# Performance work log

Hardware: AMD Instinct MI355X
Metric: run time of the kernel (lower is better)

## Reference

```python
import jax, jax.numpy as jnp
import numpy as np
from jax import lax

V = 10475
J = 55
B = 512
# Kinematic tree: hardcoded chain (parent[i] = i-1), root = 0.
PARENTS = np.concatenate([[-1], np.arange(J - 1)]).astype(np.int32)


def rodrigues(r):
    """Axis-angle (..., 3) -> rotation matrices (..., 3, 3)."""
    angle = jnp.sqrt(jnp.sum(r * r, axis=-1, keepdims=True) + 1e-12)  # (...,1)
    axis = r / angle
    s = jnp.sin(angle)[..., None]
    c = jnp.cos(angle)[..., None]
    kx, ky, kz = axis[..., 0], axis[..., 1], axis[..., 2]
    z = jnp.zeros_like(kx)
    K = jnp.stack([z, -kz, ky, kz, z, -kx, -ky, kx, z], axis=-1).reshape(r.shape[:-1] + (3, 3))
    I = jnp.eye(3, dtype=r.dtype)
    return I + s * K + (1.0 - c) * (K @ K)


def setup_inputs() -> dict:
    key = jax.random.key(0)
    ks = jax.random.split(key, 16)
    inp = {
        'shape': jax.random.normal(ks[0], (1, 10), jnp.float32),
        'body_pose': jax.random.normal(ks[1], (B, 21, 3), jnp.float32) * 0.3,
        'hand_pose': jax.random.normal(ks[2], (B, 30, 3), jnp.float32) * 0.3,
        'head_pose': jax.random.normal(ks[3], (B, 3, 3), jnp.float32) * 0.3,
        'expression': jax.random.normal(ks[4], (B, 10), jnp.float32),
        'pelvis_rotation': jax.random.normal(ks[5], (B, 3), jnp.float32) * 0.3,
        'global_translation': jax.random.normal(ks[6], (B, 3), jnp.float32),
        'v_template': jax.random.normal(ks[7], (V, 3), jnp.float32),
        'shapedirs': jax.random.normal(ks[8], (V, 3, 10), jnp.float32) * 0.01,
        'exprdirs': jax.random.normal(ks[9], (V, 3, 10), jnp.float32) * 0.01,
        'posedirs': jax.random.normal(ks[10], (486, V * 3), jnp.float32) * 0.001,
    }
    w = jax.random.uniform(ks[11], (V, J), jnp.float32)
    inp['lbs_weights'] = w / jnp.sum(w, axis=-1, keepdims=True)
    jr = jax.random.uniform(ks[12], (J, V), jnp.float32)
    inp['J_regressor'] = jr / jnp.sum(jr, axis=-1, keepdims=True)
    inp['hand_mean'] = jax.random.normal(ks[13], (2, 45), jnp.float32) * 0.1
    return inp


def reference(shape, body_pose, hand_pose, head_pose, expression, pelvis_rotation,
              global_translation, v_template, shapedirs, exprdirs, posedirs,
              lbs_weights, J_regressor, hand_mean):
    b = body_pose.shape[0]
    dtype = v_template.dtype

    # 1) shape + expression blendshapes -> (B, V, 3)
    v_shaped = (v_template[None]
                + jnp.einsum('bs,vcs->bvc', shape, shapedirs)
                + jnp.einsum('be,vce->bvc', expression, exprdirs))

    # 2) joint locations (B, J, 3)
    joints = jnp.einsum('jv,bvc->bjc', J_regressor, v_shaped)

    # 3) assemble full pose (B, 55, 3): pelvis | body(21) | head(3) | hands(30)
    hands = hand_pose.reshape(b, 90) + hand_mean.reshape(90)[None]
    full_pose = jnp.concatenate(
        [pelvis_rotation[:, None], body_pose, head_pose, hands.reshape(b, 30, 3)], axis=1)
    rotmats = rodrigues(full_pose)  # (B, J, 3, 3)

    # 4) pose blendshapes
    I3 = jnp.eye(3, dtype=dtype)
    pose_feature = (rotmats[:, 1:] - I3).reshape(b, (J - 1) * 9)  # (B, 486)
    v_posed = v_shaped + (pose_feature @ posedirs).reshape(b, V, 3)

    # 5) local joint transforms (B, J, 4, 4)
    rel_joints = joints.at[:, 1:].add(-joints[:, PARENTS[1:]])
    top = jnp.concatenate([rotmats, rel_joints[..., None]], axis=-1)  # (B,J,3,4)
    bottom = jnp.broadcast_to(
        jnp.array([0., 0., 0., 1.], dtype=dtype), (b, J, 1, 4))
    T_local = jnp.concatenate([top, bottom], axis=-2)

    # 6) compose along kinematic chain (parent[i] = i-1 -> scan)
    def step(G_prev, T_i):
        G = G_prev @ T_i  # (B,4,4)
        return G, G
    G0 = T_local[:, 0]
    _, Gs = lax.scan(step, G0, jnp.swapaxes(T_local[:, 1:], 0, 1))
    G = jnp.concatenate([G0[:, None], jnp.swapaxes(Gs, 0, 1)], axis=1)  # (B,J,4,4)

    # 7) remove rest-pose joint locations: A = G * inv(rest)
    A = G.at[..., :3, 3].add(-jnp.einsum('bjrc,bjc->bjr', G[..., :3, :3], joints))

    # 8) linear blend skinning
    T = jnp.einsum('vj,bjrc->bvrc', lbs_weights, A)  # (B,V,4,4)
    verts = jnp.einsum('bvrc,bvc->bvr', T[..., :3, :3], v_posed) + T[..., :3, 3]

    # 9) ground plane + global translation
    y_offset = -jnp.min(v_template[:, 1])
    verts = verts.at[..., 1].add(y_offset)
    verts = verts + global_translation[:, None]
    return verts
```

## Files before the change

kernel.cpp:

```cpp
#include <hip/hip_runtime.h>
#include <hip/hip_bf16.h>


typedef _Float16 f16;
typedef f16  f16x8 __attribute__((ext_vector_type(8)));
typedef f16  f16x4 __attribute__((ext_vector_type(4)));
typedef float f32x4 __attribute__((ext_vector_type(4)));

#define VN    10475
#define JN    55
#define BN    512
#define VC3   31425
#define NPAD  31488
#define VPADV 10496

#define SD_F  0
#define JS_F  31425
#define JE_F  31590
#define Y_F   33240
#define PFH_BYTE  (160*1024)
#define AH_BYTE   (768*1024)
#define VPH_BYTE  (2*1024*1024)
#define LWT_BYTE  (34*1024*1024)

#define NB_PDT  984
#define NB_SD   123
#define NB_LWT  164
#define NB_JREG 165
#define NB_PREP (NB_PDT + NB_SD + 1 + NB_LWT + NB_JREG)

#define BTS 520

__global__ __launch_bounds__(256) void k_prep(
    const float* __restrict__ vt, const float* __restrict__ shapedirs,
    const float* __restrict__ shape, const float* __restrict__ lw,
    const float* __restrict__ jr, const float* __restrict__ exprdirs,
    const float* __restrict__ pd, const float* __restrict__ ed,
    float* __restrict__ ws, f16* __restrict__ lwT, f16* __restrict__ PDH)
{
    __shared__ char SMEM[32*BTS*2];
    const int bb  = blockIdx.x;
    const int tid = threadIdx.x;

    if (bb < NB_PDT) {
        f16* Bt = (f16*)SMEM;
        const int n0 = bb * 32;
        {
            const int krow = tid >> 3;
            const int cg   = (tid & 7) * 4;
            const int nb   = n0 + cg;
            #pragma unroll 8
            for (int p = 0; p < 16; ++p) {
                int k = krow + p*32;
                float4 vv = make_float4(0.f, 0.f, 0.f, 0.f);
                if (k < 486) {
                    if (nb + 3 < VC3) vv = *(const float4*)(pd + (size_t)k*VC3 + nb);
                    else {
                        float* pv = (float*)&vv;
                        for (int e = 0; e < 4; ++e)
                            if (nb + e < VC3) pv[e] = pd[(size_t)k*VC3 + nb + e];
                    }
                } else if (k < 496) {
                    float* pv = (float*)&vv;
                    for (int e = 0; e < 4; ++e)
                        if (nb + e < VC3) pv[e] = ed[(size_t)(nb + e)*10 + (k - 486)];
                }
                Bt[(cg+0)*BTS + k] = (f16)vv.x;
                Bt[(cg+1)*BTS + k] = (f16)vv.y;
                Bt[(cg+2)*BTS + k] = (f16)vv.z;
                Bt[(cg+3)*BTS + k] = (f16)vv.w;
            }
        }
        __syncthreads();
        const int w = tid >> 6, lane = tid & 63, l = lane & 15, q = lane >> 4;
        #pragma unroll
        for (int mt = 0; mt < 2; ++mt)
            #pragma unroll
            for (int kk = 0; kk < 4; ++kk) {
                int kc = w*4 + kk;
                f16x8 vv8 = *(const f16x8*)&Bt[(mt*16 + l)*BTS + kc*32 + q*8];
                *(f16x8*)&PDH[(size_t)(2*bb + mt)*8192 + kc*512 + lane*8] = vv8;
            }
    } else if (bb < NB_PDT + NB_SD) {
        int i = (bb - NB_PDT) * 256 + tid;
        if (i < VC3) {
            float acc = vt[i];
            const float* sd = shapedirs + (size_t)i * 10;
            #pragma unroll
            for (int s = 0; s < 10; ++s) acc += shape[s] * sd[s];
            ws[SD_F + i] = acc;
        }
    } else if (bb == NB_PDT + NB_SD) {
        float* red = (float*)SMEM;
        float m = 3.0e38f;
        for (int v = tid; v < VN; v += 256) m = fminf(m, vt[v*3 + 1]);
        red[tid] = m;
        __syncthreads();
        for (int s = 128; s > 0; s >>= 1) {
            if (tid < s) red[tid] = fminf(red[tid], red[tid + s]);
            __syncthreads();
        }
        if (tid == 0) ws[Y_F] = -red[0];
    } else if (bb < NB_PDT + NB_SD + 1 + NB_LWT) {
        int bx = bb - (NB_PDT + NB_SD + 1);
        int v  = bx * 64 + (tid >> 2);
        int jg = (tid & 3) * 16;
        f16 tmp[16];
        #pragma unroll
        for (int jj = 0; jj < 16; ++jj) {
            int j = jg + jj;
            tmp[jj] = (f16)((v < VN && j < JN) ? lw[(size_t)v*JN + j] : 0.f);
        }
        int vtile = v >> 4, lv = v & 15;
        int ks = jg >> 5, q0 = (jg >> 3) & 3;
        *(f16x8*)&lwT[(size_t)vtile*1024 + ks*512 + (q0*16 + lv)*8]     = *(f16x8*)&tmp[0];
        *(f16x8*)&lwT[(size_t)vtile*1024 + ks*512 + ((q0+1)*16 + lv)*8] = *(f16x8*)&tmp[8];
    } else {
        float* red = (float*)SMEM;
        int jb = bb - (NB_PDT + NB_SD + 1 + NB_LWT);
        int j = jb / 3, c = jb % 3;
        float acc[11];
        #pragma unroll
        for (int i = 0; i < 11; ++i) acc[i] = 0.f;
        for (int v = tid; v < VN; v += 256) {
            float w = jr[(size_t)j * VN + v];
            float sv = vt[v*3 + c];
            const float* sd = shapedirs + (size_t)(v*3 + c) * 10;
            #pragma unroll
            for (int s = 0; s < 10; ++s) sv += shape[s] * sd[s];
            acc[10] += w * sv;
            const float* edp = exprdirs + (size_t)(v*3 + c) * 10;
            #pragma unroll
            for (int e = 0; e < 10; ++e) acc[e] += w * edp[e];
        }
        for (int i = 0; i < 11; ++i) {
            red[tid] = acc[i];
            __syncthreads();
            for (int s = 128; s > 0; s >>= 1) {
                if (tid < s) red[tid] += red[tid + s];
                __syncthreads();
            }
            if (tid == 0) {
                if (i == 10) ws[JS_F + j*3 + c] = red[0];
                else         ws[JE_F + (j*3 + c)*10 + i] = red[0];
            }
            __syncthreads();
        }
    }
}

__global__ void k_batch(const float* __restrict__ body, const float* __restrict__ hand,
                        const float* __restrict__ head, const float* __restrict__ expr,
                        const float* __restrict__ pelvis, const float* __restrict__ hand_mean,
                        const float* __restrict__ ws, f16* __restrict__ PFH,
                        f16* __restrict__ AH)
{
    int b = blockIdx.x, tid = threadIdx.x;
    __shared__ float rot[JN][9];
    __shared__ float jnt[JN][3];

    f16* AHb = AH + (size_t)b * 1024;
    #pragma unroll
    for (int i = 0; i < 16; ++i) AHb[tid + i*64] = (f16)0.f;

    if (tid < JN) {
        int j = tid;
        float r0, r1, r2;
        if (j == 0) {
            r0 = pelvis[b*3+0]; r1 = pelvis[b*3+1]; r2 = pelvis[b*3+2];
        } else if (j <= 21) {
            int o = b*63 + (j-1)*3;
            r0 = body[o]; r1 = body[o+1]; r2 = body[o+2];
        } else if (j <= 24) {
            int o = b*9 + (j-22)*3;
            r0 = head[o]; r1 = head[o+1]; r2 = head[o+2];
        } else {
            int h = (j-25)*3;
            r0 = hand[b*90+h+0] + hand_mean[h+0];
            r1 = hand[b*90+h+1] + hand_mean[h+1];
            r2 = hand[b*90+h+2] + hand_mean[h+2];
        }
        float a2  = r0*r0 + r1*r1 + r2*r2 + 1e-12f;
        float ang = sqrtf(a2);
        float inv = 1.0f / ang;
        float kx = r0*inv, ky = r1*inv, kz = r2*inv;
        float s = sinf(ang), c = cosf(ang), ic = 1.0f - c;
        rot[j][0] = c + ic*kx*kx;    rot[j][1] = ic*kx*ky - s*kz; rot[j][2] = ic*kx*kz + s*ky;
        rot[j][3] = ic*kx*ky + s*kz; rot[j][4] = c + ic*ky*ky;    rot[j][5] = ic*ky*kz - s*kx;
        rot[j][6] = ic*kx*kz - s*ky; rot[j][7] = ic*ky*kz + s*kx; rot[j][8] = c + ic*kz*kz;
        #pragma unroll
        for (int cc = 0; cc < 3; ++cc) {
            float acc = ws[JS_F + j*3 + cc];
            #pragma unroll
            for (int e = 0; e < 10; ++e)
                acc += expr[b*10 + e] * ws[JE_F + (j*3 + cc)*10 + e];
            jnt[j][cc] = acc;
        }
    }
    __syncthreads();

    #pragma unroll
    for (int i = 0; i < 8; ++i) {
        int k = tid + i*64;
        float val = 0.f;
        if (k < 486) {
            int jj = k/9 + 1, ii = k%9;
            float d = (ii == 0 || ii == 4 || ii == 8) ? 1.0f : 0.0f;
            val = rot[jj][ii] - d;
        } else if (k < 496) {
            val = expr[b*10 + (k-486)];
        }
        PFH[(size_t)((b>>4)*16 + (k>>5))*512 + (((k>>3)&3)*16 + (b&15))*8 + (k&7)] = (f16)val;
    }

    int r = tid >> 2, cc = tid & 3;
    float g = 0.f;
    if (tid < 12) g = (cc < 3) ? rot[0][r*3 + cc] : jnt[0][r];
    for (int j = 0; j < JN; ++j) {
        if (j > 0) {
            float g0 = __shfl(g, r*4+0), g1 = __shfl(g, r*4+1);
            float g2 = __shfl(g, r*4+2), g3 = __shfl(g, r*4+3);
            if (cc < 3) g = g0*rot[j][cc] + g1*rot[j][3+cc] + g2*rot[j][6+cc];
            else        g = g0*(jnt[j][0]-jnt[j-1][0]) + g1*(jnt[j][1]-jnt[j-1][1])
                          + g2*(jnt[j][2]-jnt[j-1][2]) + g3;
        }
        float h0 = __shfl(g, r*4+0), h1 = __shfl(g, r*4+1), h2 = __shfl(g, r*4+2);
        float aval = g;
        if (cc == 3) aval = g - (h0*jnt[j][0] + h1*jnt[j][1] + h2*jnt[j][2]);
        if (tid < 12)
            AHb[(j>>5)*512 + (((j>>3)&3)*16 + tid)*8 + (j&7)] = (f16)aval;
    }
}

__global__ __launch_bounds__(256) void k_pose(
    const float* __restrict__ ws, const f16* __restrict__ PDH,
    const f16* __restrict__ PFH, f16* __restrict__ VPH2)
{
    const int t = threadIdx.x;
    const int bx = blockIdx.x;
    const int by = blockIdx.y;
    const int n0 = bx * 64;
    const int w = t >> 6, lane = t & 63, l = lane & 15, q = lane >> 4;

    f32x4 acc[4][4];
    #pragma unroll
    for (int i = 0; i < 4; ++i)
        #pragma unroll
        for (int j = 0; j < 4; ++j) acc[i][j] = (f32x4)0.f;

    for (int kc = 0; kc < 16; ++kc) {
        f16x8 af[4], bf[4];
        #pragma unroll
        for (int mt = 0; mt < 4; ++mt)
            af[mt] = *(const f16x8*)&PDH[(size_t)(4*bx + mt)*8192 + kc*512 + lane*8];
        #pragma unroll
        for (int nt = 0; nt < 4; ++nt)
            bf[nt] = *(const f16x8*)&PFH[(size_t)((by*16 + w*4 + nt)*16 + kc)*512 + lane*8];
        #pragma unroll
        for (int mt = 0; mt < 4; ++mt)
            #pragma unroll
            for (int nt = 0; nt < 4; ++nt)
                acc[mt][nt] = __builtin_amdgcn_mfma_f32_16x16x32_f16(af[mt], bf[nt], acc[mt][nt], 0, 0, 0);
    }

    #pragma unroll
    for (int mt = 0; mt < 4; ++mt) {
        int nb2 = n0 + mt*16 + q*4;
        float sdv[4];
        #pragma unroll
        for (int i = 0; i < 4; ++i)
            sdv[i] = (nb2 + i < VC3) ? ws[SD_F + nb2 + i] : 0.f;
        #pragma unroll
        for (int nt = 0; nt < 4; ++nt) {
            int b = by*256 + w*64 + nt*16 + l;
            f16 pack[4];
            #pragma unroll
            for (int i = 0; i < 4; ++i)
                pack[i] = (f16)(acc[mt][nt][i] + sdv[i]);
            *(f16x4*)&VPH2[(size_t)b*NPAD + nb2] = *(f16x4*)&pack[0];
        }
    }
}

__global__ __launch_bounds__(256, 8) void k_lbs(
    const float* __restrict__ gt, const float* __restrict__ ws,
    const f16* __restrict__ AH, const f16* __restrict__ lwT,
    const f16* __restrict__ VPH2, float* __restrict__ out)
{
    __shared__ f16   LV[8*192];
    __shared__ float OUTS[8*192];
    const int t = threadIdx.x;
    const int v0 = blockIdx.x * 64;
    const int bbase = blockIdx.y * 8;
    const int w = t >> 6, lane = t & 63, l = lane & 15, q = lane >> 4;

    if (t < 192) {
        int bl = t / 24, c8 = t % 24;
        *(f16x8*)&LV[bl*192 + c8*8] =
            *(const f16x8*)&VPH2[(size_t)(bbase + bl)*NPAD + v0*3 + c8*8];
    }
    __syncthreads();

    f32x4 acc[2][4];
    #pragma unroll
    for (int i = 0; i < 2; ++i)
        #pragma unroll
        for (int j = 0; j < 4; ++j) acc[i][j] = (f32x4)0.f;

    #pragma unroll
    for (int ks = 0; ks < 2; ++ks) {
        f16x8 af[2], bf[4];
        #pragma unroll
        for (int nt = 0; nt < 4; ++nt)
            bf[nt] = *(const f16x8*)&lwT[(size_t)(blockIdx.x*4 + nt)*1024 + ks*512 + lane*8];
        #pragma unroll
        for (int mt = 0; mt < 2; ++mt)
            af[mt] = *(const f16x8*)&AH[(size_t)(bbase + w*2 + mt)*1024 + ks*512 + lane*8];
        #pragma unroll
        for (int mt = 0; mt < 2; ++mt)
            #pragma unroll
            for (int nt = 0; nt < 4; ++nt)
                acc[mt][nt] = __builtin_amdgcn_mfma_f32_16x16x32_f16(af[mt], bf[nt], acc[mt][nt], 0, 0, 0);
    }

    float yoff = ws[Y_F];
    #pragma unroll
    for (int mt = 0; mt < 2; ++mt) {
        int bl = w*2 + mt;
        float add = 0.f;
        if (q < 3) add = gt[(bbase + bl)*3 + q] + (q == 1 ? yoff : 0.f);
        const f16* vrow = &LV[bl*192];
        #pragma unroll
        for (int nt = 0; nt < 4; ++nt) {
            if (q < 3) {
                int o = (nt*16 + l)*3;
                float vx = (float)vrow[o], vy = (float)vrow[o+1], vz = (float)vrow[o+2];
                f32x4 T = acc[mt][nt];
                OUTS[bl*192 + o + q] = T[0]*vx + T[1]*vy + T[2]*vz + T[3] + add;
            }
        }
    }
    __syncthreads();
    #pragma unroll
    for (int pass = 0; pass < 6; ++pass) {
        int idx = pass*256 + t;
        int bl  = idx / 192;
        int c   = idx - bl*192;
        if (v0*3 + c < VC3)
            out[(size_t)(bbase + bl)*VC3 + v0*3 + c] = OUTS[idx];
    }
}

extern "C" void kernel_launch(void* const* d_in, const int* in_sizes, int n_in,
                              void* d_out, int out_size, void* d_ws, size_t ws_size,
                              hipStream_t stream)
{
    const float* shape  = (const float*)d_in[0];
    const float* body   = (const float*)d_in[1];
    const float* hand   = (const float*)d_in[2];
    const float* head   = (const float*)d_in[3];
    const float* expr   = (const float*)d_in[4];
    const float* pelvis = (const float*)d_in[5];
    const float* gtrans = (const float*)d_in[6];
    const float* vt     = (const float*)d_in[7];
    const float* shdirs = (const float*)d_in[8];
    const float* exdirs = (const float*)d_in[9];
    const float* pdirs  = (const float*)d_in[10];
    const float* lbsw   = (const float*)d_in[11];
    const float* jreg   = (const float*)d_in[12];
    const float* hmean  = (const float*)d_in[13];
    float* wsf  = (float*)d_ws;
    f16*   PFH  = (f16*)((char*)d_ws + PFH_BYTE);
    f16*   AH   = (f16*)((char*)d_ws + AH_BYTE);
    f16*   VPH2 = (f16*)((char*)d_ws + VPH_BYTE);
    f16*   lwT  = (f16*)((char*)d_ws + LWT_BYTE);
    f16*   PDH  = (f16*)d_out;
    float* out  = (float*)d_out;

    hipLaunchKernelGGL(k_prep,  dim3(NB_PREP), dim3(256), 0, stream,
                       vt, shdirs, shape, lbsw, jreg, exdirs, pdirs, exdirs, wsf, lwT, PDH);
    hipLaunchKernelGGL(k_batch, dim3(BN),   dim3(64),  0, stream,
                       body, hand, head, expr, pelvis, hmean, wsf, PFH, AH);
    hipLaunchKernelGGL(k_pose,  dim3(NPAD/64, 2), dim3(256), 0, stream,
                       wsf, PDH, PFH, VPH2);
    hipLaunchKernelGGL(k_lbs,   dim3(VPADV/64, 8192/128), dim3(256), 0, stream,
                       gtrans, wsf, AH, lwT, VPH2, out);
}
```

Baseline: 277.1 us.

## Repack posedirs into f16 MFMA tiles without shared-memory transpose

Rewrites the posedirs/exprdirs repacking branch of the prep kernel so each thread reads 8 scalar k-values for one column directly from global memory and writes one f16x8 packet to the tiled layout. This drops the 32-column LDS transpose tile and its barrier, and uses many more, smaller blocks (492x16). It trades the float4 vectorized loads for scalar, coalesced-across-lanes loads and cuts LDS use for the whole prep kernel to a 256-float reduction buffer, which may raise occupancy.

```diff
diff --git a/kernel.cpp b/kernel.cpp
--- a/kernel.cpp
+++ b/kernel.cpp
@@ -23,13 +23,11 @@
 #define VPH_BYTE  (2*1024*1024)
 #define LWT_BYTE  (34*1024*1024)
 
-#define NB_PDT  984
+#define NB_PDT  (492*16)
 #define NB_SD   123
 #define NB_LWT  164
 #define NB_JREG 165
 #define NB_PREP (NB_PDT + NB_SD + 1 + NB_LWT + NB_JREG)
-
-#define BTS 520
 
 __global__ __launch_bounds__(256) void k_prep(
     const float* __restrict__ vt, const float* __restrict__ shapedirs,
@@ -38,49 +36,29 @@
     const float* __restrict__ pd, const float* __restrict__ ed,
     float* __restrict__ ws, f16* __restrict__ lwT, f16* __restrict__ PDH)
 {
-    __shared__ char SMEM[32*BTS*2];
+    __shared__ float red[256];
     const int bb  = blockIdx.x;
     const int tid = threadIdx.x;
 
     if (bb < NB_PDT) {
-        f16* Bt = (f16*)SMEM;
-        const int n0 = bb * 32;
-        {
-            const int krow = tid >> 3;
-            const int cg   = (tid & 7) * 4;
-            const int nb   = n0 + cg;
-            #pragma unroll 8
-            for (int p = 0; p < 16; ++p) {
-                int k = krow + p*32;
-                float4 vv = make_float4(0.f, 0.f, 0.f, 0.f);
-                if (k < 486) {
-                    if (nb + 3 < VC3) vv = *(const float4*)(pd + (size_t)k*VC3 + nb);
-                    else {
-                        float* pv = (float*)&vv;
-                        for (int e = 0; e < 4; ++e)
-                            if (nb + e < VC3) pv[e] = pd[(size_t)k*VC3 + nb + e];
-                    }
-                } else if (k < 496) {
-                    float* pv = (float*)&vv;
-                    for (int e = 0; e < 4; ++e)
-                        if (nb + e < VC3) pv[e] = ed[(size_t)(nb + e)*10 + (k - 486)];
-                }
-                Bt[(cg+0)*BTS + k] = (f16)vv.x;
-                Bt[(cg+1)*BTS + k] = (f16)vv.y;
-                Bt[(cg+2)*BTS + k] = (f16)vv.z;
-                Bt[(cg+3)*BTS + k] = (f16)vv.w;
+        const int ky = bb / 492;
+        const int bx = bb - ky * 492;
+        const int n  = bx * 64 + (tid & 63);
+        const int w  = tid >> 6;
+        const int k0 = ky * 32 + w * 8;
+        f16 h[8];
+        #pragma unroll
+        for (int e = 0; e < 8; ++e) {
+            int k = k0 + e;
+            float x = 0.f;
+            if (n < VC3) {
+                if (k < 486)      x = pd[(size_t)k * VC3 + n];
+                else if (k < 496) x = ed[(size_t)n * 10 + (k - 486)];
             }
-        }
-        __syncthreads();
-        const int w = tid >> 6, lane = tid & 63, l = lane & 15, q = lane >> 4;
-        #pragma unroll
-        for (int mt = 0; mt < 2; ++mt)
-            #pragma unroll
-            for (int kk = 0; kk < 4; ++kk) {
-                int kc = w*4 + kk;
-                f16x8 vv8 = *(const f16x8*)&Bt[(mt*16 + l)*BTS + kc*32 + q*8];
-                *(f16x8*)&PDH[(size_t)(2*bb + mt)*8192 + kc*512 + lane*8] = vv8;
-            }
+            h[e] = (f16)x;
+        }
+        *(f16x8*)&PDH[(size_t)(n >> 4) * 8192 + ky * 512 + (w * 16 + (tid & 15)) * 8]
+            = *(f16x8*)&h[0];
     } else if (bb < NB_PDT + NB_SD) {
         int i = (bb - NB_PDT) * 256 + tid;
         if (i < VC3) {
@@ -91,7 +69,6 @@
             ws[SD_F + i] = acc;
         }
     } else if (bb == NB_PDT + NB_SD) {
-        float* red = (float*)SMEM;
         float m = 3.0e38f;
         for (int v = tid; v < VN; v += 256) m = fminf(m, vt[v*3 + 1]);
         red[tid] = m;
@@ -116,7 +93,6 @@
         *(f16x8*)&lwT[(size_t)vtile*1024 + ks*512 + (q0*16 + lv)*8]     = *(f16x8*)&tmp[0];
         *(f16x8*)&lwT[(size_t)vtile*1024 + ks*512 + ((q0+1)*16 + lv)*8] = *(f16x8*)&tmp[8];
     } else {
-        float* red = (float*)SMEM;
         int jb = bb - (NB_PDT + NB_SD + 1 + NB_LWT);
         int j = jb / 3, c = jb % 3;
         float acc[11];
```

Result: slower. 306.8 us (+10.7%).
